# Performance work log

Measured on AMD Instinct MI355X. Metric: run time of the kernel, lower is better.

Reference implementation:

```python
import jax, jax.numpy as jnp
import numpy as np

N_NODES = 50000
N_EDGES = 800000
HIDDEN = 128
OUT = 128


def setup_inputs() -> dict:
    key = jax.random.key(0)
    k1, k2, k3, k4, k5, k6 = jax.random.split(key, 6)
    h = jax.random.normal(k1, (N_NODES, HIDDEN), dtype=jnp.float32)
    src = jax.random.randint(k2, (N_EDGES,), 0, N_NODES, dtype=jnp.int64)
    dst = jax.random.randint(k3, (N_EDGES,), 0, N_NODES, dtype=jnp.int64)
    scale = 1.0 / np.sqrt(HIDDEN)
    W_edge = jax.random.normal(k4, (OUT, HIDDEN), dtype=jnp.float32) * scale
    W_self = jax.random.normal(k5, (OUT, HIDDEN), dtype=jnp.float32) * scale
    b_self = jax.random.normal(k6, (OUT,), dtype=jnp.float32) * scale
    return {"h": h, "src": src, "dst": dst, "W_edge": W_edge, "W_self": W_self, "b_self": b_self}


def reference(h, src, dst, W_edge, W_self, b_self):
    n = h.shape[0]
    # edge_transform(src_features): same linear on every edge -> transform nodes once, then gather
    msg_node = h @ W_edge.T                       # [N, OUT]
    msg = msg_node[src]                           # [E, OUT] gather
    sums = jax.ops.segment_sum(msg, dst, num_segments=n)  # [N, OUT] scatter-add
    deg = jax.ops.segment_sum(jnp.ones((dst.shape[0],), dtype=h.dtype), dst, num_segments=n)
    h1 = sums / jnp.maximum(deg, 1.0)[:, None]    # mean; zero in-degree -> 0 (DGL semantics)
    out = jax.nn.relu(h @ W_self.T + b_self + h1)
    return out
```

## Files before the change

kernel.cpp:

```cpp
#include <hip/hip_runtime.h>

#define N_HID 128
#define CAP   32
#define OVF_CAP 8192
#define NSLICE 8
#define PBLK   256

typedef short bf16x8 __attribute__((ext_vector_type(8)));
typedef float f32x4  __attribute__((ext_vector_type(4)));

static __device__ __forceinline__ unsigned short f2bf(float f)
{
    unsigned int u = __float_as_uint(f);
    u = (u + 0x7fffu + ((u >> 16) & 1u)) >> 16;
    return (unsigned short)u;
}
static __device__ __forceinline__ unsigned int pack2(float a, float b)
{
    return (unsigned int)f2bf(a) | ((unsigned int)f2bf(b) << 16);
}
static __device__ __forceinline__ float bf2f(unsigned int bits16)
{
    return __uint_as_float(bits16 << 16);
}
static __device__ __forceinline__ int slice_of(int d, float sln)
{
    int sl = (int)((float)d * sln);
    return sl > NSLICE - 1 ? NSLICE - 1 : sl;
}

__global__ __launch_bounds__(256) void count_fragw_cast(
    const int* __restrict__ dst, int* __restrict__ blockCnt,
    int* __restrict__ cnt, int* __restrict__ ovfn, int E, int n, float sln,
    const float* __restrict__ We, const float* __restrict__ Ws,
    unsigned short* __restrict__ Be, unsigned short* __restrict__ Bs,
    const float* __restrict__ h, unsigned short* __restrict__ hbf, int total)
{
    int t = threadIdx.x, b = blockIdx.x;

    if (b >= PBLK + 16) {
        int idx = (b - PBLK - 16) * 2048 + t * 8;
        if (idx + 8 <= total) {
            float4 v0 = *(const float4*)&h[idx];
            float4 v1 = *(const float4*)&h[idx + 4];
            uint4 pk;
            pk.x = pack2(v0.x, v0.y);
            pk.y = pack2(v0.z, v0.w);
            pk.z = pack2(v1.x, v1.y);
            pk.w = pack2(v1.z, v1.w);
            *(uint4*)&hbf[idx] = pk;
        }
        return;
    }

    if (b >= PBLK) {
        int bb = b - PBLK;
        const float* srcw = (bb < 8) ? We : Ws;
        unsigned short* dstF = (bb < 8) ? Be : Bs;
        int rt = bb & 7;
        int kc = t >> 6, l = t & 63, m = l & 15, q = l >> 4;
        const float* p = &srcw[(size_t)(rt * 16 + m) * N_HID + kc * 32 + q * 8];
        float4 v0 = *(const float4*)p;
        float4 v1 = *(const float4*)(p + 4);
        uint4 pk;
        pk.x = pack2(v0.x, v0.y);
        pk.y = pack2(v0.z, v0.w);
        pk.z = pack2(v1.x, v1.y);
        pk.w = pack2(v1.z, v1.w);
        *(uint4*)&dstF[(size_t)rt * 2048 + kc * 512 + l * 8] = pk;
        return;
    }

    for (int i = b * 256 + t; i < n; i += PBLK * 256) cnt[i] = 0;
    if (b == 0 && t == 0) *ovfn = 0;

    int c[NSLICE];
#pragma unroll
    for (int s = 0; s < NSLICE; ++s) c[s] = 0;

    for (int e = b * 256 + t; e < E; e += PBLK * 256) {
        int sl = slice_of(dst[e], sln);
#pragma unroll
        for (int s = 0; s < NSLICE; ++s) c[s] += (sl == s);
    }

    __shared__ int red[NSLICE * 4];
    int lane = t & 63, wid = t >> 6;
#pragma unroll
    for (int s = 0; s < NSLICE; ++s) {
        int v = c[s];
#pragma unroll
        for (int off = 32; off; off >>= 1) v += __shfl_down(v, off);
        if (lane == 0) red[s * 4 + wid] = v;
    }
    __syncthreads();
    if (t < NSLICE)
        blockCnt[t * PBLK + b] = red[t*4+0] + red[t*4+1] + red[t*4+2] + red[t*4+3];
}

__global__ __launch_bounds__(256) void part_scan(
    const int* __restrict__ blockCnt, int* __restrict__ blockBase,
    int* __restrict__ sbase, int E)
{
    __shared__ int wsm[4];
    int t = threadIdx.x, lane = t & 63, wid = t >> 6;
    int v[8]; int s = 0;
#pragma unroll
    for (int i = 0; i < 8; ++i) { v[i] = blockCnt[t * 8 + i]; s += v[i]; }
    int val = s;
#pragma unroll
    for (int off = 1; off < 64; off <<= 1) {
        int y = __shfl_up(val, off);
        if (lane >= off) val += y;
    }
    if (lane == 63) wsm[wid] = val;
    __syncthreads();
    if (t == 0) { int a = 0; for (int w = 0; w < 4; ++w) { int tmp = wsm[w]; wsm[w] = a; a += tmp; } }
    __syncthreads();
    int excl = wsm[wid] + val - s;
#pragma unroll
    for (int i = 0; i < 8; ++i) { int tv = v[i]; blockBase[t * 8 + i] = excl; excl += tv; }
    __syncthreads();
    if (t < NSLICE) sbase[t] = blockBase[t * PBLK];
    if (t == 0)     sbase[NSLICE] = E;
}

__global__ __launch_bounds__(256) void part_scatter(
    const int* __restrict__ src, const int* __restrict__ dst,
    const int* __restrict__ blockBase, unsigned int* __restrict__ part,
    int E, int n, float sln)
{
    __shared__ int cur[NSLICE];
    int t = threadIdx.x, b = blockIdx.x;
    if (t < NSLICE) cur[t] = blockBase[t * PBLK + b];
    __syncthreads();
    for (int e = b * 256 + t; e < E; e += PBLK * 256) {
        int d = dst[e], s = src[e];
        int sl  = slice_of(d, sln);
        int pos = atomicAdd(&cur[sl], 1);
        part[pos] = ((unsigned int)d << 16) | (unsigned int)s;
    }
}

__global__ __launch_bounds__(256) void bucket_scatter2(
    const unsigned int* __restrict__ part,
    const int* __restrict__ sbase,
    int* __restrict__ cnt,
    unsigned short* __restrict__ bucket,
    int* __restrict__ ovfn,
    long long* __restrict__ ovf)
{
    const int slice = blockIdx.x & 7;
    const int g     = blockIdx.x >> 3;
    const int nG    = (int)(gridDim.x >> 3);
    const int lo    = sbase[slice];
    const int hi    = sbase[slice + 1];
    const int m     = hi - lo;

    const int chunk = (m + nG - 1) / nG;
    const int e0 = lo + g * chunk;
    int e1 = e0 + chunk; if (e1 > hi) e1 = hi;

    for (int e = e0 + (int)threadIdx.x; e < e1; e += 256) {
        unsigned int pk = part[e];
        int d = (int)(pk >> 16);
        int s = (int)(pk & 0xffffu);
        int c = atomicAdd(&cnt[d], 1);
        if (c < CAP) {
            bucket[(size_t)d * CAP + c] = (unsigned short)s;
        } else {
            int o = atomicAdd(ovfn, 1);
            if (o < OVF_CAP) ovf[o] = ((long long)d << 32) | (unsigned int)s;
        }
    }
}

__global__ __launch_bounds__(256) void gather_mean(
    const int* __restrict__ cnt,
    const unsigned short* __restrict__ bucket,
    const int* __restrict__ ovfn,
    const long long* __restrict__ ovf,
    const unsigned short* __restrict__ hbf,
    unsigned short* __restrict__ hagg,
    int n, float sln)
{
    const int slice = blockIdx.x & 7;
    const int g     = blockIdx.x >> 3;
    const int lo    = (int)(((long long)slice * n) / NSLICE);
    const int hi    = (int)(((long long)(slice + 1) * n) / NSLICE);
    int node = lo + g * 4 + ((int)threadIdx.x >> 6);
    if (node >= hi) return;

    int lane = threadIdx.x & 63;
    int deg  = cnt[node];
    int m    = deg < CAP ? deg : CAP;

    const unsigned short* bk = &bucket[(size_t)node * CAP];
    const unsigned int* h32 = (const unsigned int*)hbf;

    float ax = 0.f, ay = 0.f;
    int i = 0;
    for (; i + 4 <= m; i += 4) {
        ushort4 ss = *(const ushort4*)&bk[i];
        unsigned int v0 = h32[(size_t)ss.x * 64 + lane];
        unsigned int v1 = h32[(size_t)ss.y * 64 + lane];
        unsigned int v2 = h32[(size_t)ss.z * 64 + lane];
        unsigned int v3 = h32[(size_t)ss.w * 64 + lane];
        ax += bf2f(v0 & 0xffffu) + bf2f(v1 & 0xffffu) + bf2f(v2 & 0xffffu) + bf2f(v3 & 0xffffu);
        ay += bf2f(v0 >> 16)     + bf2f(v1 >> 16)     + bf2f(v2 >> 16)     + bf2f(v3 >> 16);
    }
    for (; i < m; ++i) {
        unsigned int v = h32[(size_t)bk[i] * 64 + lane];
        ax += bf2f(v & 0xffffu);
        ay += bf2f(v >> 16);
    }

    if (deg > CAP) {
        int no = *ovfn; if (no > OVF_CAP) no = OVF_CAP;
        for (int o = 0; o < no; ++o) {
            long long pk = ovf[o];
            if ((int)(pk >> 32) == node) {
                unsigned int v = h32[(size_t)(unsigned int)pk * 64 + lane];
                ax += bf2f(v & 0xffffu);
                ay += bf2f(v >> 16);
            }
        }
    }

    float sc = deg > 0 ? 1.0f / (float)deg : 0.f;

    int rt = node >> 4, mm = node & 15;
    int kc = lane >> 4, q = (lane >> 2) & 3, j = (lane & 3) * 2;
    unsigned int pk = pack2(ax * sc, ay * sc);
    *(unsigned int*)&hagg[(size_t)rt * 2048 + kc * 512 + (q * 16 + mm) * 8 + j] = pk;
}

__global__ __launch_bounds__(256) void gemm_final(
    const unsigned short* __restrict__ hbf,
    const unsigned short* __restrict__ hagg,
    const unsigned short* __restrict__ Be,
    const unsigned short* __restrict__ Bsf,
    const float* __restrict__ bias,
    float* __restrict__ out,
    int n, int nrt)
{
    int w = (int)((blockIdx.x * blockDim.x + threadIdx.x) >> 6);
    if (w >= nrt) return;
    int l = threadIdx.x & 63;
    int m = l & 15, q = l >> 4;
    int row0 = w * 16;

    bf16x8 ah[4];
#pragma unroll
    for (int kc = 0; kc < 4; ++kc) {
        int gr = row0 + m; if (gr > n - 1) gr = n - 1;
        ah[kc] = *(const bf16x8*)&hbf[(size_t)gr * N_HID + kc * 32 + q * 8];
    }
    const bf16x8* Gp = (const bf16x8*)(hagg + (size_t)w * 2048);
    bf16x8 ag0 = Gp[l], ag1 = Gp[64 + l], ag2 = Gp[128 + l], ag3 = Gp[192 + l];

    const int colb = l & 15;
    const int rq   = (l >> 4) * 4;

#pragma unroll
    for (int ct = 0; ct < 8; ++ct) {
        const bf16x8* BpS = (const bf16x8*)(Bsf + (size_t)ct * 2048);
        const bf16x8* BpE = (const bf16x8*)(Be  + (size_t)ct * 2048);
        f32x4 acc = {0.f, 0.f, 0.f, 0.f};
        acc = __builtin_amdgcn_mfma_f32_16x16x32_bf16(ah[0], BpS[l],       acc, 0, 0, 0);
        acc = __builtin_amdgcn_mfma_f32_16x16x32_bf16(ah[1], BpS[64 + l],  acc, 0, 0, 0);
        acc = __builtin_amdgcn_mfma_f32_16x16x32_bf16(ah[2], BpS[128 + l], acc, 0, 0, 0);
        acc = __builtin_amdgcn_mfma_f32_16x16x32_bf16(ah[3], BpS[192 + l], acc, 0, 0, 0);
        acc = __builtin_amdgcn_mfma_f32_16x16x32_bf16(ag0,   BpE[l],       acc, 0, 0, 0);
        acc = __builtin_amdgcn_mfma_f32_16x16x32_bf16(ag1,   BpE[64 + l],  acc, 0, 0, 0);
        acc = __builtin_amdgcn_mfma_f32_16x16x32_bf16(ag2,   BpE[128 + l], acc, 0, 0, 0);
        acc = __builtin_amdgcn_mfma_f32_16x16x32_bf16(ag3,   BpE[192 + l], acc, 0, 0, 0);

        int col = ct * 16 + colb;
        float bv = bias[col];
#pragma unroll
        for (int r = 0; r < 4; ++r) {
            int row = row0 + rq + r;
            if (row < n) out[(size_t)row * N_HID + col] = fmaxf(acc[r] + bv, 0.f);
        }
    }
}

extern "C" void kernel_launch(void* const* d_in, const int* in_sizes, int n_in,
                              void* d_out, int out_size, void* d_ws, size_t ws_size,
                              hipStream_t stream)
{
    const float* h   = (const float*)d_in[0];
    const int*   src = (const int*)d_in[1];
    const int*   dst = (const int*)d_in[2];
    const float* We  = (const float*)d_in[3];
    const float* Ws  = (const float*)d_in[4];
    const float* bs  = (const float*)d_in[5];
    float*       out = (float*)d_out;

    const int n   = in_sizes[0] / N_HID;
    const int E   = in_sizes[1];
    const int nrt = (n + 15) / 16;
    const float sln = (float)NSLICE / (float)n;
    const int total = n * N_HID;

    unsigned short* hbf  = (unsigned short*)d_ws;
    unsigned short* hagg = hbf + (size_t)n * N_HID;
    unsigned short* bucket = hagg + (size_t)nrt * 2048;
    unsigned short* Be  = bucket + (size_t)n * CAP;
    unsigned short* Bs  = Be + 8 * 2048;
    int*  cnt  = (int*)(Bs + 8 * 2048);
    int*  ovfn = cnt + n;
    long long* ovf = (long long*)(ovfn + 8);
    int*  blockCnt  = (int*)(ovf + OVF_CAP);
    int*  blockBase = blockCnt + PBLK * NSLICE;
    int*  sbase     = blockBase + PBLK * NSLICE;
    unsigned int* part = (unsigned int*)(sbase + 16);

    const int castBlocks = (total + 2047) / 2048;
    const int nodeBlocksPerSlice = ((n / NSLICE) + 4) / 4 + 1;

    count_fragw_cast<<<PBLK + 16 + castBlocks, 256, 0, stream>>>(
        dst, blockCnt, cnt, ovfn, E, n, sln, We, Ws, Be, Bs, h, hbf, total);
    part_scan<<<1, 256, 0, stream>>>(blockCnt, blockBase, sbase, E);
    part_scatter<<<PBLK, 256, 0, stream>>>(src, dst, blockBase, part, E, n, sln);
    bucket_scatter2<<<1024, 256, 0, stream>>>(part, sbase, cnt, bucket, ovfn, ovf);
    gather_mean<<<8 * nodeBlocksPerSlice, 256, 0, stream>>>(cnt, bucket, ovfn, ovf,
                                                            hbf, hagg, n, sln);
    gemm_final<<<(nrt + 3) / 4, 256, 0, stream>>>(hbf, hagg, Be, Bs, bs, out, n, nrt);
}
```

Baseline: 187.2 us.

## Fuse neighbor mean gather with final MFMA GEMM through LDS tiles

Merges the gather_mean and gemm_final kernels into one. Each wave now gathers 16 consecutive nodes serially, packs their means into a padded LDS tile, and feeds that tile straight into the MFMA GEMM. This drops the hagg round-trip through global memory and one kernel launch, and unrolls the bucket loop to 8 loads. In exchange each wave walks 16 nodes in sequence, so there are 16x fewer waves in the gather phase and less memory-level parallelism for the random loads.

New measurement: 199.5 us. +6.6%, slower.

```diff
diff --git a/kernel.cpp b/kernel.cpp
--- a/kernel.cpp
+++ b/kernel.cpp
@@ -175,106 +175,130 @@
     }
 }
 
-__global__ __launch_bounds__(256) void gather_mean(
+__global__ __launch_bounds__(256) void gather_gemm(
     const int* __restrict__ cnt,
     const unsigned short* __restrict__ bucket,
     const int* __restrict__ ovfn,
     const long long* __restrict__ ovf,
     const unsigned short* __restrict__ hbf,
-    unsigned short* __restrict__ hagg,
-    int n, float sln)
-{
-    const int slice = blockIdx.x & 7;
-    const int g     = blockIdx.x >> 3;
-    const int lo    = (int)(((long long)slice * n) / NSLICE);
-    const int hi    = (int)(((long long)(slice + 1) * n) / NSLICE);
-    int node = lo + g * 4 + ((int)threadIdx.x >> 6);
-    if (node >= hi) return;
-
-    int lane = threadIdx.x & 63;
-    int deg  = cnt[node];
-    int m    = deg < CAP ? deg : CAP;
-
-    const unsigned short* bk = &bucket[(size_t)node * CAP];
-    const unsigned int* h32 = (const unsigned int*)hbf;
-
-    float ax = 0.f, ay = 0.f;
-    int i = 0;
-    for (; i + 4 <= m; i += 4) {
-        ushort4 ss = *(const ushort4*)&bk[i];
-        unsigned int v0 = h32[(size_t)ss.x * 64 + lane];
-        unsigned int v1 = h32[(size_t)ss.y * 64 + lane];
-        unsigned int v2 = h32[(size_t)ss.z * 64 + lane];
-        unsigned int v3 = h32[(size_t)ss.w * 64 + lane];
-        ax += bf2f(v0 & 0xffffu) + bf2f(v1 & 0xffffu) + bf2f(v2 & 0xffffu) + bf2f(v3 & 0xffffu);
-        ay += bf2f(v0 >> 16)     + bf2f(v1 >> 16)     + bf2f(v2 >> 16)     + bf2f(v3 >> 16);
-    }
-    for (; i < m; ++i) {
-        unsigned int v = h32[(size_t)bk[i] * 64 + lane];
-        ax += bf2f(v & 0xffffu);
-        ay += bf2f(v >> 16);
-    }
-
-    if (deg > CAP) {
-        int no = *ovfn; if (no > OVF_CAP) no = OVF_CAP;
-        for (int o = 0; o < no; ++o) {
-            long long pk = ovf[o];
-            if ((int)(pk >> 32) == node) {
-                unsigned int v = h32[(size_t)(unsigned int)pk * 64 + lane];
-                ax += bf2f(v & 0xffffu);
-                ay += bf2f(v >> 16);
-            }
-        }
-    }
-
-    float sc = deg > 0 ? 1.0f / (float)deg : 0.f;
-
-    int rt = node >> 4, mm = node & 15;
-    int kc = lane >> 4, q = (lane >> 2) & 3, j = (lane & 3) * 2;
-    unsigned int pk = pack2(ax * sc, ay * sc);
-    *(unsigned int*)&hagg[(size_t)rt * 2048 + kc * 512 + (q * 16 + mm) * 8 + j] = pk;
-}
-
-__global__ __launch_bounds__(256) void gemm_final(
-    const unsigned short* __restrict__ hbf,
-    const unsigned short* __restrict__ hagg,
     const unsigned short* __restrict__ Be,
     const unsigned short* __restrict__ Bsf,
     const float* __restrict__ bias,
     float* __restrict__ out,
     int n, int nrt)
 {
-    int w = (int)((blockIdx.x * blockDim.x + threadIdx.x) >> 6);
-    if (w >= nrt) return;
-    int l = threadIdx.x & 63;
-    int m = l & 15, q = l >> 4;
-    int row0 = w * 16;
-
-    bf16x8 ah[4];
+    __shared__ __align__(16) unsigned int lds[4 * 16 * 68];
+
+    const int t    = threadIdx.x;
+    const int wid  = t >> 6;
+    const int lane = t & 63;
+    const int slice = blockIdx.x & 7;
+    const int g     = blockIdx.x >> 3;
+    const int tLo = (int)(((long long)slice * nrt) >> 3);
+    const int tHi = (int)(((long long)(slice + 1) * nrt) >> 3);
+    const int tile = tLo + g * 4 + wid;
+    const bool active = tile < tHi;
+
+    unsigned int* wl = &lds[wid * (16 * 68)];
+    const unsigned int* h32 = (const unsigned int*)hbf;
+
+    if (active) {
+        for (int mm = 0; mm < 16; ++mm) {
+            int node = tile * 16 + mm;
+            float ax = 0.f, ay = 0.f;
+            if (node < n) {
+                int deg = cnt[node];
+                int m = deg < CAP ? deg : CAP;
+                const unsigned short* bk = &bucket[(size_t)node * CAP];
+
+                int i = 0;
+                for (; i + 8 <= m; i += 8) {
+                    uint4 b4 = *(const uint4*)&bk[i];
+                    unsigned int r0 = b4.x & 0xffffu, r1 = b4.x >> 16;
+                    unsigned int r2 = b4.y & 0xffffu, r3 = b4.y >> 16;
+                    unsigned int r4 = b4.z & 0xffffu, r5 = b4.z >> 16;
+                    unsigned int r6 = b4.w & 0xffffu, r7 = b4.w >> 16;
+                    unsigned int v0 = h32[(size_t)r0 * 64 + lane];
+                    unsigned int v1 = h32[(size_t)r1 * 64 + lane];
+                    unsigned int v2 = h32[(size_t)r2 * 64 + lane];
+                    unsigned int v3 = h32[(size_t)r3 * 64 + lane];
+                    unsigned int v4 = h32[(size_t)r4 * 64 + lane];
+                    unsigned int v5 = h32[(size_t)r5 * 64 + lane];
+                    unsigned int v6 = h32[(size_t)r6 * 64 + lane];
+                    unsigned int v7 = h32[(size_t)r7 * 64 + lane];
+                    ax += bf2f(v0 & 0xffffu) + bf2f(v1 & 0xffffu)
+                        + bf2f(v2 & 0xffffu) + bf2f(v3 & 0xffffu)
+                        + bf2f(v4 & 0xffffu) + bf2f(v5 & 0xffffu)
+                        + bf2f(v6 & 0xffffu) + bf2f(v7 & 0xffffu);
+                    ay += bf2f(v0 >> 16) + bf2f(v1 >> 16)
+                        + bf2f(v2 >> 16) + bf2f(v3 >> 16)
+                        + bf2f(v4 >> 16) + bf2f(v5 >> 16)
+                        + bf2f(v6 >> 16) + bf2f(v7 >> 16);
+                }
+                for (; i + 4 <= m; i += 4) {
+                    ushort4 ss = *(const ushort4*)&bk[i];
+                    unsigned int v0 = h32[(size_t)ss.x * 64 + lane];
+                    unsigned int v1 = h32[(size_t)ss.y * 64 + lane];
+                    unsigned int v2 = h32[(size_t)ss.z * 64 + lane];
+                    unsigned int v3 = h32[(size_t)ss.w * 64 + lane];
+                    ax += bf2f(v0 & 0xffffu) + bf2f(v1 & 0xffffu)
+                        + bf2f(v2 & 0xffffu) + bf2f(v3 & 0xffffu);
+                    ay += bf2f(v0 >> 16) + bf2f(v1 >> 16)
+                        + bf2f(v2 >> 16) + bf2f(v3 >> 16);
+                }
+                for (; i < m; ++i) {
+                    unsigned int v = h32[(size_t)bk[i] * 64 + lane];
+                    ax += bf2f(v & 0xffffu);
+                    ay += bf2f(v >> 16);
+                }
+
+                if (deg > CAP) {
+                    int no = *ovfn; if (no > OVF_CAP) no = OVF_CAP;
+                    for (int o = 0; o < no; ++o) {
+                        long long pk = ovf[o];
+                        if ((int)(pk >> 32) == node) {
+                            unsigned int v = h32[(size_t)(unsigned int)pk * 64 + lane];
+                            ax += bf2f(v & 0xffffu);
+                            ay += bf2f(v >> 16);
+                        }
+                    }
+                }
+                float sc = deg > 0 ? 1.0f / (float)deg : 0.f;
+                ax *= sc; ay *= sc;
+            }
+            wl[mm * 68 + lane] = pack2(ax, ay);
+        }
+    }
+    __syncthreads();
+    if (!active) return;
+
+    const int rr = lane & 15, q = lane >> 4;
+    const int row0 = tile * 16;
+
+    bf16x8 ah[4], ag[4];
 #pragma unroll
     for (int kc = 0; kc < 4; ++kc) {
-        int gr = row0 + m; if (gr > n - 1) gr = n - 1;
+        int gr = row0 + rr; if (gr > n - 1) gr = n - 1;
         ah[kc] = *(const bf16x8*)&hbf[(size_t)gr * N_HID + kc * 32 + q * 8];
-    }
-    const bf16x8* Gp = (const bf16x8*)(hagg + (size_t)w * 2048);
-    bf16x8 ag0 = Gp[l], ag1 = Gp[64 + l], ag2 = Gp[128 + l], ag3 = Gp[192 + l];
-
-    const int colb = l & 15;
-    const int rq   = (l >> 4) * 4;
+        ag[kc] = *(const bf16x8*)&wl[rr * 68 + kc * 16 + q * 4];
+    }
+
+    const int colb = lane & 15;
+    const int rq   = (lane >> 4) * 4;
 
 #pragma unroll
     for (int ct = 0; ct < 8; ++ct) {
         const bf16x8* BpS = (const bf16x8*)(Bsf + (size_t)ct * 2048);
         const bf16x8* BpE = (const bf16x8*)(Be  + (size_t)ct * 2048);
         f32x4 acc = {0.f, 0.f, 0.f, 0.f};
-        acc = __builtin_amdgcn_mfma_f32_16x16x32_bf16(ah[0], BpS[l],       acc, 0, 0, 0);
-        acc = __builtin_amdgcn_mfma_f32_16x16x32_bf16(ah[1], BpS[64 + l],  acc, 0, 0, 0);
-        acc = __builtin_amdgcn_mfma_f32_16x16x32_bf16(ah[2], BpS[128 + l], acc, 0, 0, 0);
-        acc = __builtin_amdgcn_mfma_f32_16x16x32_bf16(ah[3], BpS[192 + l], acc, 0, 0, 0);
-        acc = __builtin_amdgcn_mfma_f32_16x16x32_bf16(ag0,   BpE[l],       acc, 0, 0, 0);
-        acc = __builtin_amdgcn_mfma_f32_16x16x32_bf16(ag1,   BpE[64 + l],  acc, 0, 0, 0);
-        acc = __builtin_amdgcn_mfma_f32_16x16x32_bf16(ag2,   BpE[128 + l], acc, 0, 0, 0);
-        acc = __builtin_amdgcn_mfma_f32_16x16x32_bf16(ag3,   BpE[192 + l], acc, 0, 0, 0);
+        acc = __builtin_amdgcn_mfma_f32_16x16x32_bf16(ah[0], BpS[lane],       acc, 0, 0, 0);
+        acc = __builtin_amdgcn_mfma_f32_16x16x32_bf16(ah[1], BpS[64 + lane],  acc, 0, 0, 0);
+        acc = __builtin_amdgcn_mfma_f32_16x16x32_bf16(ah[2], BpS[128 + lane], acc, 0, 0, 0);
+        acc = __builtin_amdgcn_mfma_f32_16x16x32_bf16(ah[3], BpS[192 + lane], acc, 0, 0, 0);
+        acc = __builtin_amdgcn_mfma_f32_16x16x32_bf16(ag[0], BpE[lane],       acc, 0, 0, 0);
+        acc = __builtin_amdgcn_mfma_f32_16x16x32_bf16(ag[1], BpE[64 + lane],  acc, 0, 0, 0);
+        acc = __builtin_amdgcn_mfma_f32_16x16x32_bf16(ag[2], BpE[128 + lane], acc, 0, 0, 0);
+        acc = __builtin_amdgcn_mfma_f32_16x16x32_bf16(ag[3], BpE[192 + lane], acc, 0, 0, 0);
 
         int col = ct * 16 + colb;
         float bv = bias[col];
@@ -305,8 +329,7 @@
     const int total = n * N_HID;
 
     unsigned short* hbf  = (unsigned short*)d_ws;
-    unsigned short* hagg = hbf + (size_t)n * N_HID;
-    unsigned short* bucket = hagg + (size_t)nrt * 2048;
+    unsigned short* bucket = hbf + (size_t)n * N_HID;
     unsigned short* Be  = bucket + (size_t)n * CAP;
     unsigned short* Bs  = Be + 8 * 2048;
     int*  cnt  = (int*)(Bs + 8 * 2048);
@@ -318,14 +341,16 @@
     unsigned int* part = (unsigned int*)(sbase + 16);
 
     const int castBlocks = (total + 2047) / 2048;
-    const int nodeBlocksPerSlice = ((n / NSLICE) + 4) / 4 + 1;
+
+    const int maxTilesPerSlice = (nrt + NSLICE - 1) / NSLICE;
+    const int blocksPerSlice   = (maxTilesPerSlice + 3) / 4;
+    const int ggGrid = NSLICE * blocksPerSlice;
 
     count_fragw_cast<<<PBLK + 16 + castBlocks, 256, 0, stream>>>(
         dst, blockCnt, cnt, ovfn, E, n, sln, We, Ws, Be, Bs, h, hbf, total);
     part_scan<<<1, 256, 0, stream>>>(blockCnt, blockBase, sbase, E);
     part_scatter<<<PBLK, 256, 0, stream>>>(src, dst, blockBase, part, E, n, sln);
     bucket_scatter2<<<1024, 256, 0, stream>>>(part, sbase, cnt, bucket, ovfn, ovf);
-    gather_mean<<<8 * nodeBlocksPerSlice, 256, 0, stream>>>(cnt, bucket, ovfn, ovf,
-                                                            hbf, hagg, n, sln);
-    gemm_final<<<(nrt + 3) / 4, 256, 0, stream>>>(hbf, hagg, Be, Bs, bs, out, n, nrt);
-}
+    gather_gemm<<<ggGrid, 256, 0, stream>>>(cnt, bucket, ovfn, ovf,
+                                            hbf, Be, Bs, bs, out, n, nrt);
+}
```
